# Kernel tuning notes

Measured on AMD Instinct MI355X. Metric: run time of the kernel, lower is better.

The kernel has to match this reference:

```python
import jax, jax.numpy as jnp
import numpy as np

IN_CH, SKIP_CH, OUT_CH = 256, 128, 128
K2 = 9  # 3x3 deformable kernel
LK = 15  # large kernel for offset conv
EPS = 1e-5


def conv2d(x, w, b, pad):
    out = jax.lax.conv_general_dilated(
        x, w, (1, 1), ((pad[0], pad[0]), (pad[1], pad[1])),
        dimension_numbers=("NCHW", "OIHW", "NCHW"))
    return out + b[None, :, None, None]


def conv_transpose_2x2_s2(x, w, b):
    # torch ConvTranspose2d(k=2, s=2, pad=0); w: [in, out, 2, 2]
    wt = jnp.flip(w, (2, 3)).transpose(1, 0, 2, 3)  # [out, in, 2, 2]
    out = jax.lax.conv_general_dilated(
        x, wt, (1, 1), ((1, 1), (1, 1)), lhs_dilation=(2, 2),
        dimension_numbers=("NCHW", "OIHW", "NCHW"))
    return out + b[None, :, None, None]


def bn_relu(x, g, b):
    # training-mode BatchNorm2d (batch statistics) + ReLU
    m = jnp.mean(x, (0, 2, 3), keepdims=True)
    v = jnp.var(x, (0, 2, 3), keepdims=True)
    xn = (x - m) * jax.lax.rsqrt(v + EPS)
    return jax.nn.relu(xn * g[None, :, None, None] + b[None, :, None, None])


def deform_conv3x3(x, offset, mask, w):
    # torchvision DeformConv2d semantics, k=3, stride=1, pad=1, dil=1, no bias
    B, C, H, W = x.shape
    off = offset.reshape(B, K2, 2, H, W)
    dy, dx = off[:, :, 0], off[:, :, 1]            # [B, 9, H, W]
    ki = (jnp.arange(K2) // 3).astype(x.dtype)
    kj = (jnp.arange(K2) % 3).astype(x.dtype)
    hh = jnp.arange(H, dtype=x.dtype)
    ww = jnp.arange(W, dtype=x.dtype)
    y = dy + (hh[None, :, None] + ki[:, None, None] - 1.0)[None]   # [B,9,H,W]
    xx = dx + (ww[None, None, :] + kj[:, None, None] - 1.0)[None]
    y0 = jnp.floor(y)
    x0 = jnp.floor(xx)
    wy = y - y0   # bilinear weights
    wx = xx - x0
    y0i = y0.astype(jnp.int32)
    x0i = x0.astype(jnp.int32)
    x_flat = x.reshape(B, C, H * W)

    def gather(yc, xc):
        valid = ((yc >= 0) & (yc < H) & (xc >= 0) & (xc < W)).astype(x.dtype)
        idx = jnp.clip(yc, 0, H - 1) * W + jnp.clip(xc, 0, W - 1)
        g = jnp.take_along_axis(x_flat, idx.reshape(B, 1, -1), axis=2)
        return g.reshape(B, C, K2, H, W) * valid[:, None]

    v00 = gather(y0i, x0i)
    v01 = gather(y0i, x0i + 1)
    v10 = gather(y0i + 1, x0i)
    v11 = gather(y0i + 1, x0i + 1)
    wye = wy[:, None]
    wxe = wx[:, None]
    sampled = (v00 * (1 - wye) * (1 - wxe) + v01 * (1 - wye) * wxe
               + v10 * wye * (1 - wxe) + v11 * wye * wxe)
    sampled = sampled * mask[:, None]              # [B,C,9,H,W]
    return jnp.einsum("bckhw,ock->bohw", sampled, w.reshape(w.shape[0], C, K2))


def setup_inputs() -> dict:
    key = jax.random.key(0)
    ks = jax.random.split(key, 16)
    s = 0.02
    return {
        "x": jax.random.normal(ks[0], (2, IN_CH, 64, 64), jnp.float32),
        "skip": jax.random.normal(ks[1], (2, SKIP_CH, 128, 128), jnp.float32),
        "w_up": jax.random.normal(ks[2], (IN_CH, OUT_CH, 2, 2), jnp.float32) * s,
        "b_up": jnp.zeros((OUT_CH,), jnp.float32),
        "w_ref": jax.random.normal(ks[3], (OUT_CH, OUT_CH + SKIP_CH, 3, 3), jnp.float32) * s,
        "b_ref": jnp.zeros((OUT_CH,), jnp.float32),
        "g1": jnp.ones((OUT_CH,), jnp.float32),
        "be1": jnp.zeros((OUT_CH,), jnp.float32),
        "w_offh": jax.random.normal(ks[4], (2 * K2, OUT_CH, 1, LK), jnp.float32) * s,
        "b_offh": jnp.zeros((2 * K2,), jnp.float32),
        "w_offv": jax.random.normal(ks[5], (2 * K2, OUT_CH, LK, 1), jnp.float32) * s,
        "b_offv": jnp.zeros((2 * K2,), jnp.float32),
        "w_mask": jax.random.normal(ks[6], (K2, OUT_CH, 3, 3), jnp.float32) * s,
        "b_mask": jnp.zeros((K2,), jnp.float32),
        "w_def": jax.random.normal(ks[7], (OUT_CH, OUT_CH, 3, 3), jnp.float32) * s,
        "g2": jnp.ones((OUT_CH,), jnp.float32),
        "be2": jnp.zeros((OUT_CH,), jnp.float32),
    }


def reference(x, skip, w_up, b_up, w_ref, b_ref, g1, be1,
              w_offh, b_offh, w_offv, b_offv, w_mask, b_mask,
              w_def, g2, be2):
    xu = conv_transpose_2x2_s2(x, w_up, b_up)            # [B, out_ch, 2H, 2W]
    cat = jnp.concatenate([xu, skip], axis=1)
    h = bn_relu(conv2d(cat, w_ref, b_ref, (1, 1)), g1, be1)
    # DSConv: LDoffset = conv(1x15) + conv(15x1); sigmoid mask; deform conv; BN+ReLU
    offset = conv2d(h, w_offh, b_offh, (0, LK // 2)) + conv2d(h, w_offv, b_offv, (LK // 2, 0))
    mask = jax.nn.sigmoid(conv2d(h, w_mask, b_mask, (1, 1)))
    return bn_relu(deform_conv3x3(h, offset, mask, w_def), g2, be2)
```

## Files before the change

### kernel.cpp

```cpp
#include <hip/hip_runtime.h>
#include <hip/hip_bf16.h>

typedef __attribute__((ext_vector_type(8))) short bf16x8;
typedef __attribute__((ext_vector_type(4))) float f32x4;
typedef __attribute__((ext_vector_type(8))) unsigned short u16x8;

static __device__ __forceinline__ unsigned short f2bf(float f) {
  union { float f; unsigned u; } v; v.f = f;
  unsigned r = v.u + 0x7fff + ((v.u >> 16) & 1);
  return (unsigned short)(r >> 16);
}

__global__ void k_wupA(const float* __restrict__ wu, unsigned short* __restrict__ wupA) {
  int idx = blockIdx.x * 256 + threadIdx.x;
  int ic = idx & 255, oc = (idx >> 8) & 127, tap = idx >> 15;
  wupA[idx] = f2bf(wu[(ic * 128 + oc) * 4 + tap]);
}

__global__ __launch_bounds__(256, 2)
void k_upsampleM(const float* __restrict__ x, const unsigned short* __restrict__ wupA,
                 const float* __restrict__ b_up, unsigned short* __restrict__ catT) {
  int bid = blockIdx.x;
  int half = bid & 1;
  int hh = (bid >> 1) & 63;
  int b  = bid >> 7;
  int ww0 = half * 32;
  int t = threadIdx.x;
  int l = t & 63, w = t >> 6;
  int kh = w >> 1, kw = w & 1;
  int lan15 = l & 15, lhi = l >> 4;
  __shared__ unsigned short xs[32][264];

  {
    int ic = t;
    const float4* xp = (const float4*)(x + (((long)(b * 256 + ic)) << 12) + (hh << 6) + ww0);
    #pragma unroll
    for (int q = 0; q < 8; ++q) {
      float4 v = xp[q];
      xs[q * 4 + 0][ic] = f2bf(v.x);
      xs[q * 4 + 1][ic] = f2bf(v.y);
      xs[q * 4 + 2][ic] = f2bf(v.z);
      xs[q * 4 + 3][ic] = f2bf(v.w);
    }
  }
  __syncthreads();

  f32x4 acc[8][2];
  #pragma unroll
  for (int m = 0; m < 8; ++m)
    #pragma unroll
    for (int n = 0; n < 2; ++n)
      #pragma unroll
      for (int r = 0; r < 4; ++r) acc[m][n][r] = 0.f;

  const unsigned short* ab = wupA + ((w * 128 + lan15) << 8) + lhi * 8;
  #pragma unroll
  for (int kc = 0; kc < 8; ++kc) {
    bf16x8 b0 = *(const bf16x8*)(&xs[lan15][kc * 32 + lhi * 8]);
    bf16x8 b1 = *(const bf16x8*)(&xs[16 + lan15][kc * 32 + lhi * 8]);
    #pragma unroll
    for (int mt = 0; mt < 8; ++mt) {
      bf16x8 af = *(const bf16x8*)(ab + (mt << 12) + kc * 32);
      acc[mt][0] = __builtin_amdgcn_mfma_f32_16x16x32_bf16(af, b0, acc[mt][0], 0, 0, 0);
      acc[mt][1] = __builtin_amdgcn_mfma_f32_16x16x32_bf16(af, b1, acc[mt][1], 0, 0, 0);
    }
  }

  int oh = 2 * hh + kh;
  #pragma unroll
  for (int mt = 0; mt < 8; ++mt) {
    int ocb = mt * 16 + lhi * 4;
    float4 bias = *(const float4*)(b_up + ocb);
    int cg = ocb >> 5, icl = ocb & 31;
    long plane = ((long)(b * 8 + cg) << 14) + (oh << 7);
    #pragma unroll
    for (int nt = 0; nt < 2; ++nt) {
      int ow = 2 * (ww0 + nt * 16 + lan15) + kw;
      unsigned u0 = (unsigned)f2bf(acc[mt][nt][0] + bias.x)
                  | ((unsigned)f2bf(acc[mt][nt][1] + bias.y) << 16);
      unsigned u1 = (unsigned)f2bf(acc[mt][nt][2] + bias.z)
                  | ((unsigned)f2bf(acc[mt][nt][3] + bias.w) << 16);
      uint2 pk; pk.x = u0; pk.y = u1;
      *(uint2*)(catT + ((plane + ow) << 5) + icl) = pk;
    }
  }
}

__global__ void k_skipT(const float* __restrict__ skip, unsigned short* __restrict__ catT) {
  int bid = blockIdx.x;
  int xb = bid & 1;
  int y  = (bid >> 1) & 127;
  int cg = (bid >> 8) & 3;
  int b  = bid >> 10;
  int t = threadIdx.x;
  __shared__ float ts[32][65];
  int x = t & 63, c4 = t >> 6, x0 = xb * 64;
  #pragma unroll
  for (int p = 0; p < 8; ++p) {
    int c = p * 4 + c4;
    ts[c][x] = skip[(((long)(b * 128 + cg * 32 + c)) << 14) + (y << 7) + x0 + x];
  }
  __syncthreads();
  int ic = t & 31, xg = t >> 5;
  long plane = ((long)(b * 8 + 4 + cg) << 14) + (y << 7) + x0;
  #pragma unroll
  for (int q = 0; q < 8; ++q) {
    int xx = xg * 8 + q;
    catT[((plane + xx) << 5) + ic] = f2bf(ts[ic][xx]);
  }
}

__global__ void k_wrefT(const float* __restrict__ wr, unsigned short* __restrict__ wbT) {
  int idx = blockIdx.x * 256 + threadIdx.x;
  int tap = idx >> 15;
  int rem = idx & 32767;
  int oc = rem >> 8, ic = rem & 255;
  wbT[idx] = f2bf(wr[(oc * 256 + ic) * 9 + tap]);
}

__global__ void k_womT(const float* __restrict__ wh, const float* __restrict__ wv,
                       const float* __restrict__ wm, unsigned short* __restrict__ wOM) {
  int idx = blockIdx.x * 256 + threadIdx.x;
  int tap = idx / 6144;
  int rem = idx - tap * 6144;
  int j = rem >> 7, ic = rem & 127;
  float v = 0.f;
  if (tap < 15) {
    if (j < 18) v = wh[(j * 128 + ic) * 15 + tap];
  } else if (tap < 30) {
    if (j < 18) v = wv[(j * 128 + ic) * 15 + (tap - 15)];
  } else {
    if (j >= 18 && j < 27) v = wm[((j - 18) * 128 + ic) * 9 + (tap - 30)];
  }
  wOM[idx] = f2bf(v);
}

__global__ void k_wdefA(const float* __restrict__ wd, unsigned short* __restrict__ wdefA) {
  int idx = blockIdx.x * 256 + threadIdx.x;
  if (idx >= 147456) return;
  int j   = idx & 7;
  int oc  = (idx >> 3) & 127;
  int lhi = (idx >> 10) & 3;
  int ks  = idx >> 12;
  int k = ks % 9, cg = ks / 9;
  int c = cg * 32 + lhi * 8 + j;
  wdefA[idx] = f2bf(wd[(oc * 128 + c) * 9 + k]);
}

__global__ __launch_bounds__(512, 2)
void k_conv3w(const unsigned short* __restrict__ catT, const unsigned short* __restrict__ wbT,
              const float* __restrict__ br, float* __restrict__ out) {
  int bid = blockIdx.x;
  int swz = (bid & 7) * 32 + (bid >> 3);
  int y = swz & 127, b = swz >> 7;
  int t = threadIdx.x;
  int l = t & 63, w = t >> 6;
  int ocg = w & 3, xh = w >> 2;
  int oc0 = ocg * 32, px0 = xh * 64;
  int lan15 = l & 15, lhi = l >> 4;
  __shared__ unsigned short xs[3 * 130 * 40];
  const u16x8 z = {0, 0, 0, 0, 0, 0, 0, 0};
  f32x4 acc[2][4];
  #pragma unroll
  for (int m = 0; m < 2; ++m)
    #pragma unroll
    for (int n = 0; n < 4; ++n)
      #pragma unroll
      for (int r = 0; r < 4; ++r) acc[m][n][r] = 0.f;
  const unsigned short* catb = catT + ((long)b << 22);

  #pragma unroll
  for (int it = 0; it < 4; ++it) {
    int idx = it * 512 + t;
    if (idx < 1560) {
      int g = idx & 3, rc = idx >> 2;
      int r = rc / 130, c = rc - r * 130;
      int gy = y + r - 1, gx = c - 1;
      u16x8 v = z;
      if ((unsigned)gy < 128u && (unsigned)gx < 128u)
        v = *(const u16x8*)(catb + (((long)(gy << 7) + gx) << 5) + g * 8);
      *(u16x8*)(xs + (r * 130 + c) * 40 + g * 8) = v;
    }
  }
  __syncthreads();

  for (int cg = 0; cg < 8; ++cg) {
    u16x8 pre[4];
    if (cg < 7) {
      #pragma unroll
      for (int it = 0; it < 4; ++it) {
        int idx = it * 512 + t;
        pre[it] = z;
        if (idx < 1560) {
          int g = idx & 3, rc = idx >> 2;
          int r = rc / 130, c = rc - r * 130;
          int gy = y + r - 1, gx = c - 1;
          if ((unsigned)gy < 128u && (unsigned)gx < 128u)
            pre[it] = *(const u16x8*)(catb + ((((long)(cg + 1) << 14) + (gy << 7) + gx) << 5) + g * 8);
        }
      }
    }
    bf16x8 af[2][9];
    #pragma unroll
    for (int mt = 0; mt < 2; ++mt)
      #pragma unroll
      for (int tap = 0; tap < 9; ++tap)
        af[mt][tap] = *(const bf16x8*)(wbT + ((tap * 128 + oc0 + mt * 16 + lan15) << 8) + cg * 32 + lhi * 8);
    #pragma unroll
    for (int tap = 0; tap < 9; ++tap) {
      int ky = tap / 3, kx = tap % 3;
      #pragma unroll
      for (int nt = 0; nt < 4; ++nt) {
        int c = px0 + nt * 16 + lan15 + kx;
        bf16x8 bfv = *(const bf16x8*)(xs + (ky * 130 + c) * 40 + lhi * 8);
        acc[0][nt] = __builtin_amdgcn_mfma_f32_16x16x32_bf16(af[0][tap], bfv, acc[0][nt], 0, 0, 0);
        acc[1][nt] = __builtin_amdgcn_mfma_f32_16x16x32_bf16(af[1][tap], bfv, acc[1][nt], 0, 0, 0);
      }
    }
    __syncthreads();
    if (cg < 7) {
      #pragma unroll
      for (int it = 0; it < 4; ++it) {
        int idx = it * 512 + t;
        if (idx < 1560) {
          int g = idx & 3, rc = idx >> 2;
          int r = rc / 130, c = rc - r * 130;
          *(u16x8*)(xs + (r * 130 + c) * 40 + g * 8) = pre[it];
        }
      }
      __syncthreads();
    }
  }

  #pragma unroll
  for (int mt = 0; mt < 2; ++mt)
    #pragma unroll
    for (int reg = 0; reg < 4; ++reg) {
      int oc = oc0 + mt * 16 + lhi * 4 + reg;
      float bias = br[oc];
      long obase = ((long)(b * 128 + oc) << 14) + (y << 7) + px0;
      #pragma unroll
      for (int nt = 0; nt < 4; ++nt)
        out[obase + nt * 16 + lan15] = acc[mt][nt][reg] + bias;
    }
}

__global__ void k_bnstats(const float* __restrict__ src, float* __restrict__ mean,
                          float* __restrict__ rstd) {
  int c = blockIdx.x, t = threadIdx.x;
  float s = 0.f, s2 = 0.f;
  for (int b = 0; b < 2; ++b) {
    const float4* p4 = (const float4*)(src + ((long)(b * 128 + c) << 14));
    for (int i = t; i < 4096; i += 256) {
      float4 v = p4[i];
      s  += v.x + v.y + v.z + v.w;
      s2 += v.x * v.x + v.y * v.y + v.z * v.z + v.w * v.w;
    }
  }
  #pragma unroll
  for (int off = 32; off; off >>= 1) {
    s  += __shfl_down(s, off);
    s2 += __shfl_down(s2, off);
  }
  __shared__ float as[4], as2[4];
  int wid = t >> 6;
  if ((t & 63) == 0) { as[wid] = s; as2[wid] = s2; }
  __syncthreads();
  if (t == 0) {
    float S = as[0] + as[1] + as[2] + as[3];
    float S2 = as2[0] + as2[1] + as2[2] + as2[3];
    float m = S / 32768.f;
    float var = S2 / 32768.f - m * m;
    mean[c] = m;
    rstd[c] = rsqrtf(var + 1e-5f);
  }
}

__global__ void k_bnrelu2(const float* __restrict__ tmp1, const float* __restrict__ mean,
                          const float* __restrict__ rstd, const float* __restrict__ g,
                          const float* __restrict__ be, unsigned short* __restrict__ hbufT) {
  int bid = blockIdx.x;
  int xb = bid & 1;
  int y  = (bid >> 1) & 127;
  int cg = (bid >> 8) & 3;
  int b  = bid >> 10;
  int t = threadIdx.x;
  __shared__ float ts[32][65];
  int x = t & 63, c4 = t >> 6, x0 = xb * 64;
  #pragma unroll
  for (int p = 0; p < 8; ++p) {
    int c = p * 4 + c4;
    int ch = cg * 32 + c;
    float sc = rstd[ch] * g[ch];
    float bb = be[ch] - mean[ch] * sc;
    long idx = ((long)(b * 128 + ch) << 14) + (y << 7) + x0 + x;
    ts[c][x] = fmaxf(tmp1[idx] * sc + bb, 0.f);
  }
  __syncthreads();
  int ic = t & 31, xg = t >> 5;
  long plane = ((long)(b * 4 + cg) << 14) + (y << 7) + x0;
  #pragma unroll
  for (int q = 0; q < 8; ++q) {
    int xx = xg * 8 + q;
    hbufT[((plane + xx) << 5) + ic] = f2bf(ts[ic][xx]);
  }
}

__global__ __launch_bounds__(256, 2)
void k_offmasks(const unsigned short* __restrict__ hbufT, const unsigned short* __restrict__ wOM,
                const float* __restrict__ bh, const float* __restrict__ bv,
                const float* __restrict__ bm,
                float* __restrict__ off, float* __restrict__ msk) {
  int bid = blockIdx.x;
  int swz = (bid & 7) * 64 + (bid >> 3);
  int b   = swz >> 8;
  int px0 = (swz & 255) * 64;
  int t = threadIdx.x;
  int l = t & 63, w = t >> 6;
  int lan15 = l & 15, lhi = l >> 4;
  int px = px0 + w * 16;
  int y = px >> 7, x0 = px & 127;
  int x = x0 + lan15;

  __shared__ unsigned short As[4 * 32 * 128];

  f32x4 acc0, acc1;
  #pragma unroll
  for (int r = 0; r < 4; ++r) { acc0[r] = 0.f; acc1[r] = 0.f; }

  const unsigned short* hb = hbufT + ((long)b << 21);
  const u16x8 z = {0, 0, 0, 0, 0, 0, 0, 0};

  for (int grp = 0; grp < 10; ++grp) {
    int tap0 = grp * 4;
    __syncthreads();
    #pragma unroll
    for (int it = 0; it < 8; ++it) {
      int i = it * 256 + t;
      int tl = i >> 9, rem = i & 511;
      int j = rem >> 4, g16 = rem & 15;
      int tap = tap0 + tl;
      u16x8 v = z;
      if (tap < 39) v = *(const u16x8*)(wOM + ((tap * 48 + j) << 7) + g16 * 8);
      *(u16x8*)(As + tl * 4096 + j * 128 + ((g16 ^ (j & 7)) << 3)) = v;
    }
    __syncthreads();
    #pragma unroll
    for (int tl = 0; tl < 4; ++tl) {
      int tap = tap0 + tl;
      if (tap < 39) {
        int ky = (tap < 15) ? 0 : ((tap < 30) ? (tap - 22) : ((tap - 30) / 3 - 1));
        int kx = (tap < 15) ? (tap - 7) : ((tap < 30) ? 0 : ((tap - 30) % 3 - 1));
        int gy = y + ky, gx = x + kx;
        bool valid = ((unsigned)gy < 128u) & ((unsigned)gx < 128u);
        const unsigned short* bp = hb + ((((long)(gy << 7) + gx) << 5) + lhi * 8);
        bool do0 = tap < 30;
        const unsigned short* a0base = As + tl * 4096 + lan15 * 128;
        const unsigned short* a1base = a0base + 16 * 128;
        #pragma unroll
        for (int cg = 0; cg < 4; ++cg) {
          u16x8 bv8 = valid ? *(const u16x8*)(bp + ((long)cg << 19)) : z;
          bf16x8 bf = (bf16x8)bv8;
          int aoff = (((cg << 2) + lhi) ^ (lan15 & 7)) << 3;
          acc1 = __builtin_amdgcn_mfma_f32_16x16x32_bf16(*(const bf16x8*)(a1base + aoff),
                                                         bf, acc1, 0, 0, 0);
          if (do0)
            acc0 = __builtin_amdgcn_mfma_f32_16x16x32_bf16(*(const bf16x8*)(a0base + aoff),
                                                           bf, acc0, 0, 0, 0);
        }
      }
    }
  }

  int sp = (y << 7) + x;
  #pragma unroll
  for (int reg = 0; reg < 4; ++reg) {
    int j0 = lhi * 4 + reg;
    off[((long)(b * 18 + j0) << 14) + sp] = acc0[reg] + bh[j0] + bv[j0];
    int j1 = 16 + lhi * 4 + reg;
    float v = acc1[reg];
    if (j1 < 18) {
      off[((long)(b * 18 + j1) << 14) + sp] = v + bh[j1] + bv[j1];
    } else if (j1 < 27) {
      int jm = j1 - 18;
      msk[((long)(b * 9 + jm) << 14) + sp] = 1.f / (1.f + expf(-(v + bm[jm])));
    }
  }
}

__global__ __launch_bounds__(256, 2)
void k_deformm(const unsigned short* __restrict__ hbufT, const float* __restrict__ off,
               const float* __restrict__ msk, const unsigned short* __restrict__ wdefA,
               float* __restrict__ out) {
  int bid = blockIdx.x;
  int xt = bid & 3;
  int h  = (bid >> 2) & 127;
  int b  = bid >> 9;
  int w0 = xt * 32;
  int t = threadIdx.x;
  int l = t & 63, w = t >> 6;
  int lan15 = l & 15, lhi = l >> 4;

  __shared__ __align__(16) unsigned short S[9][32][40];
  __shared__ int   p_y0[288], p_x0[288];
  __shared__ float p_w00[288], p_w01[288], p_w10[288], p_w11[288];

  for (int idx = t; idx < 288; idx += 256) {
    int k = idx >> 5, pix = idx & 31;
    int sp = (h << 7) + w0 + pix;
    float dy = off[((long)(b * 18 + 2 * k) << 14) + sp];
    float dx = off[((long)(b * 18 + 2 * k + 1) << 14) + sp];
    float m  = msk[((long)(b * 9 + k) << 14) + sp];
    float y  = dy + (float)(h + k / 3 - 1);
    float xx = dx + (float)(w0 + pix + (k % 3) - 1);
    float y0f = floorf(y), x0f = floorf(xx);
    float wy = y - y0f, wx = xx - x0f;
    p_y0[idx] = (int)y0f; p_x0[idx] = (int)x0f;
    p_w00[idx] = (1.f - wy) * (1.f - wx) * m;
    p_w01[idx] = (1.f - wy) * wx * m;
    p_w10[idx] = wy * (1.f - wx) * m;
    p_w11[idx] = wy * wx * m;
  }

  f32x4 acc[2][2];
  #pragma unroll
  for (int m = 0; m < 2; ++m)
    #pragma unroll
    for (int n = 0; n < 2; ++n)
      #pragma unroll
      for (int r = 0; r < 4; ++r) acc[m][n][r] = 0.f;

  for (int cg = 0; cg < 4; ++cg) {
    __syncthreads();
    const unsigned short* hb = hbufT + (((long)(b * 4 + cg)) << 19);
    for (int idx = t; idx < 1152; idx += 256) {
      int cq = idx & 3, pix = (idx >> 2) & 31, k = idx >> 7;
      int kp = (k << 5) + pix;
      int y0 = p_y0[kp], x0 = p_x0[kp];
      float c00 = p_w00[kp], c01 = p_w01[kp], c10 = p_w10[kp], c11 = p_w11[kp];
      bool yi0 = (unsigned)y0 < 128u, yi1 = (unsigned)(y0 + 1) < 128u;
      bool xi0 = (unsigned)x0 < 128u, xi1 = (unsigned)(x0 + 1) < 128u;
      const unsigned short* pbase = hb + ((((long)(y0 << 7) + x0) << 5) + cq * 8);
      u16x8 z = {0, 0, 0, 0, 0, 0, 0, 0};
      u16x8 v00 = (yi0 && xi0) ? *(const u16x8*)pbase          : z;
      u16x8 v01 = (yi0 && xi1) ? *(const u16x8*)(pbase + 32)   : z;
      u16x8 v10 = (yi1 && xi0) ? *(const u16x8*)(pbase + 4096) : z;
      u16x8 v11 = (yi1 && xi1) ? *(const u16x8*)(pbase + 4128) : z;
      u16x8 o;
      #pragma unroll
      for (int j = 0; j < 8; ++j) {
        float s = c00 * __uint_as_float((unsigned)(unsigned short)v00[j] << 16)
                + c01 * __uint_as_float((unsigned)(unsigned short)v01[j] << 16)
                + c10 * __uint_as_float((unsigned)(unsigned short)v10[j] << 16)
                + c11 * __uint_as_float((unsigned)(unsigned short)v11[j] << 16);
        o[j] = f2bf(s);
      }
      *(u16x8*)(&S[k][pix][cq * 8]) = o;
    }
    bf16x8 af0[9], af1[9];
    #pragma unroll
    for (int k = 0; k < 9; ++k) {
      long wbase = ((((long)(cg * 9 + k) * 4 + lhi) * 128) + w * 32 + lan15) * 8;
      af0[k] = *(const bf16x8*)(wdefA + wbase);
      af1[k] = *(const bf16x8*)(wdefA + wbase + 128);
    }
    __syncthreads();
    #pragma unroll
    for (int k = 0; k < 9; ++k) {
      #pragma unroll
      for (int nt = 0; nt < 2; ++nt) {
        bf16x8 bfv = *(const bf16x8*)(&S[k][nt * 16 + lan15][lhi * 8]);
        acc[0][nt] = __builtin_amdgcn_mfma_f32_16x16x32_bf16(af0[k], bfv, acc[0][nt], 0, 0, 0);
        acc[1][nt] = __builtin_amdgcn_mfma_f32_16x16x32_bf16(af1[k], bfv, acc[1][nt], 0, 0, 0);
      }
    }
  }
  #pragma unroll
  for (int mt = 0; mt < 2; ++mt)
    #pragma unroll
    for (int reg = 0; reg < 4; ++reg) {
      int oc = w * 32 + mt * 16 + lhi * 4 + reg;
      long obase = ((long)(b * 128 + oc) << 14) + (h << 7) + w0;
      out[obase + lan15]      = acc[mt][0][reg];
      out[obase + 16 + lan15] = acc[mt][1][reg];
    }
}

__global__ void k_bnrelu(const float4* __restrict__ src, const float* __restrict__ mean,
                         const float* __restrict__ rstd, const float* __restrict__ g,
                         const float* __restrict__ be, float4* __restrict__ dst) {
  int i = blockIdx.x * 256 + threadIdx.x;
  if (i >= 1048576) return;
  int c = (i >> 12) & 127;
  float sc = rstd[c] * g[c];
  float bb = be[c] - mean[c] * sc;
  float4 v = src[i];
  v.x = fmaxf(v.x * sc + bb, 0.f);
  v.y = fmaxf(v.y * sc + bb, 0.f);
  v.z = fmaxf(v.z * sc + bb, 0.f);
  v.w = fmaxf(v.w * sc + bb, 0.f);
  dst[i] = v;
}

extern "C" void kernel_launch(void* const* d_in, const int* in_sizes, int n_in,
                              void* d_out, int out_size, void* d_ws, size_t ws_size,
                              hipStream_t stream) {
  const float* x      = (const float*)d_in[0];
  const float* skip   = (const float*)d_in[1];
  const float* w_up   = (const float*)d_in[2];
  const float* b_up   = (const float*)d_in[3];
  const float* w_ref  = (const float*)d_in[4];
  const float* b_ref  = (const float*)d_in[5];
  const float* g1     = (const float*)d_in[6];
  const float* be1    = (const float*)d_in[7];
  const float* w_offh = (const float*)d_in[8];
  const float* b_offh = (const float*)d_in[9];
  const float* w_offv = (const float*)d_in[10];
  const float* b_offv = (const float*)d_in[11];
  const float* w_mask = (const float*)d_in[12];
  const float* b_mask = (const float*)d_in[13];
  const float* w_def  = (const float*)d_in[14];
  const float* g2     = (const float*)d_in[15];
  const float* be2    = (const float*)d_in[16];

  char* W = (char*)d_ws;
  unsigned short* catT  = (unsigned short*)W;
  float*          tmp1  = (float*)(W + 16777216);
  unsigned short* hbufT = (unsigned short*)(W + 33554432);
  float*          offb  = (float*)(W + 41943040);
  float*          mskb  = (float*)(W + 44302336);
  float*          stat  = (float*)(W + 45481984);
  unsigned short* wbT   = (unsigned short*)(W + 45484032);
  unsigned short* wOM   = (unsigned short*)(W + 46073856);
  unsigned short* wdefA = (unsigned short*)(W + 46553088);
  unsigned short* wupA  = (unsigned short*)(W + 46848000);
  float*          dpre  = (float*)W;

  hipLaunchKernelGGL(k_wrefT, dim3(1152), dim3(256), 0, stream, w_ref, wbT);
  hipLaunchKernelGGL(k_womT, dim3(936), dim3(256), 0, stream, w_offh, w_offv, w_mask, wOM);
  hipLaunchKernelGGL(k_wdefA, dim3(576), dim3(256), 0, stream, w_def, wdefA);
  hipLaunchKernelGGL(k_wupA, dim3(512), dim3(256), 0, stream, w_up, wupA);
  hipLaunchKernelGGL(k_upsampleM, dim3(256), dim3(256), 0, stream, x, wupA, b_up, catT);
  hipLaunchKernelGGL(k_skipT, dim3(2048), dim3(256), 0, stream, skip, catT);
  hipLaunchKernelGGL(k_conv3w, dim3(256), dim3(512), 0, stream, catT, wbT, b_ref, tmp1);
  hipLaunchKernelGGL(k_bnstats, dim3(128), dim3(256), 0, stream, tmp1, stat, stat + 128);
  hipLaunchKernelGGL(k_bnrelu2, dim3(2048), dim3(256), 0, stream, tmp1, stat, stat + 128,
                     g1, be1, hbufT);
  hipLaunchKernelGGL(k_offmasks, dim3(512), dim3(256), 0, stream, hbufT, wOM,
                     b_offh, b_offv, b_mask, offb, mskb);
  hipLaunchKernelGGL(k_deformm, dim3(1024), dim3(256), 0, stream, hbufT, offb, mskb,
                     wdefA, dpre);
  hipLaunchKernelGGL(k_bnstats, dim3(128), dim3(256), 0, stream, dpre, stat + 256, stat + 384);
  hipLaunchKernelGGL(k_bnrelu, dim3(4096), dim3(256), 0, stream,
                     (const float4*)dpre, stat + 256, stat + 384, g2, be2, (float4*)d_out);
}
```

Measured before the change: 184.9 us.

## Split 3x3 refine conv along input channels into two partial-sum outputs

The refine conv kernel now splits the 256 input channels into two halves, launching 512 blocks instead of 256. Each half writes its partial sum to a separate buffer, and the bias is added only in the first half. The BN stats and BN+ReLU kernels are changed to read and sum both partials. The goal is to fill more CUs on the device, since 256 blocks likely underused the GPU. The cost is an extra 16MB fp32 buffer that must be written and then read twice.

```diff
diff --git a/kernel.cpp b/kernel.cpp
--- a/kernel.cpp
+++ b/kernel.cpp
@@ -148,11 +148,14 @@
 }
 
 __global__ __launch_bounds__(512, 2)
-void k_conv3w(const unsigned short* __restrict__ catT, const unsigned short* __restrict__ wbT,
-              const float* __restrict__ br, float* __restrict__ out) {
+void k_conv3s(const unsigned short* __restrict__ catT, const unsigned short* __restrict__ wbT,
+              const float* __restrict__ br, float* __restrict__ out0, float* __restrict__ out1) {
   int bid = blockIdx.x;
-  int swz = (bid & 7) * 32 + (bid >> 3);
-  int y = swz & 127, b = swz >> 7;
+  int swz = (bid & 7) * 64 + (bid >> 3);
+  int kh = swz & 1;
+  int y  = (swz >> 1) & 127;
+  int b  = swz >> 8;
+  int cg0 = kh * 4;
   int t = threadIdx.x;
   int l = t & 63, w = t >> 6;
   int ocg = w & 3, xh = w >> 2;
@@ -178,15 +181,16 @@
       int gy = y + r - 1, gx = c - 1;
       u16x8 v = z;
       if ((unsigned)gy < 128u && (unsigned)gx < 128u)
-        v = *(const u16x8*)(catb + (((long)(gy << 7) + gx) << 5) + g * 8);
+        v = *(const u16x8*)(catb + ((((long)cg0 << 14) + (gy << 7) + gx) << 5) + g * 8);
       *(u16x8*)(xs + (r * 130 + c) * 40 + g * 8) = v;
     }
   }
   __syncthreads();
 
-  for (int cg = 0; cg < 8; ++cg) {
+  for (int ci = 0; ci < 4; ++ci) {
+    int cg = cg0 + ci;
     u16x8 pre[4];
-    if (cg < 7) {
+    if (ci < 3) {
       #pragma unroll
       for (int it = 0; it < 4; ++it) {
         int idx = it * 512 + t;
@@ -218,7 +222,7 @@
       }
     }
     __syncthreads();
-    if (cg < 7) {
+    if (ci < 3) {
       #pragma unroll
       for (int it = 0; it < 4; ++it) {
         int idx = it * 512 + t;
@@ -232,12 +236,13 @@
     }
   }
 
+  float* out = kh ? out1 : out0;
   #pragma unroll
   for (int mt = 0; mt < 2; ++mt)
     #pragma unroll
     for (int reg = 0; reg < 4; ++reg) {
       int oc = oc0 + mt * 16 + lhi * 4 + reg;
-      float bias = br[oc];
+      float bias = kh ? 0.f : br[oc];
       long obase = ((long)(b * 128 + oc) << 14) + (y << 7) + px0;
       #pragma unroll
       for (int nt = 0; nt < 4; ++nt)
@@ -245,16 +250,18 @@
     }
 }
 
-__global__ void k_bnstats(const float* __restrict__ src, float* __restrict__ mean,
-                          float* __restrict__ rstd) {
+__global__ void k_bnstats2(const float* __restrict__ srcA, const float* __restrict__ srcB,
+                           float* __restrict__ mean, float* __restrict__ rstd) {
   int c = blockIdx.x, t = threadIdx.x;
   float s = 0.f, s2 = 0.f;
   for (int b = 0; b < 2; ++b) {
-    const float4* p4 = (const float4*)(src + ((long)(b * 128 + c) << 14));
+    const float4* pa = (const float4*)(srcA + ((long)(b * 128 + c) << 14));
+    const float4* pb = (const float4*)(srcB + ((long)(b * 128 + c) << 14));
     for (int i = t; i < 4096; i += 256) {
-      float4 v = p4[i];
-      s  += v.x + v.y + v.z + v.w;
-      s2 += v.x * v.x + v.y * v.y + v.z * v.z + v.w * v.w;
+      float4 va = pa[i], vb = pb[i];
+      float x0 = va.x + vb.x, x1 = va.y + vb.y, x2 = va.z + vb.z, x3 = va.w + vb.w;
+      s  += x0 + x1 + x2 + x3;
+      s2 += x0 * x0 + x1 * x1 + x2 * x2 + x3 * x3;
     }
   }
   #pragma unroll
@@ -276,9 +283,41 @@
   }
 }
 
-__global__ void k_bnrelu2(const float* __restrict__ tmp1, const float* __restrict__ mean,
-                          const float* __restrict__ rstd, const float* __restrict__ g,
-                          const float* __restrict__ be, unsigned short* __restrict__ hbufT) {
+__global__ void k_bnstats(const float* __restrict__ src, float* __restrict__ mean,
+                          float* __restrict__ rstd) {
+  int c = blockIdx.x, t = threadIdx.x;
+  float s = 0.f, s2 = 0.f;
+  for (int b = 0; b < 2; ++b) {
+    const float4* p4 = (const float4*)(src + ((long)(b * 128 + c) << 14));
+    for (int i = t; i < 4096; i += 256) {
+      float4 v = p4[i];
+      s  += v.x + v.y + v.z + v.w;
+      s2 += v.x * v.x + v.y * v.y + v.z * v.z + v.w * v.w;
+    }
+  }
+  #pragma unroll
+  for (int off = 32; off; off >>= 1) {
+    s  += __shfl_down(s, off);
+    s2 += __shfl_down(s2, off);
+  }
+  __shared__ float as[4], as2[4];
+  int wid = t >> 6;
+  if ((t & 63) == 0) { as[wid] = s; as2[wid] = s2; }
+  __syncthreads();
+  if (t == 0) {
+    float S = as[0] + as[1] + as[2] + as[3];
+    float S2 = as2[0] + as2[1] + as2[2] + as2[3];
+    float m = S / 32768.f;
+    float var = S2 / 32768.f - m * m;
+    mean[c] = m;
+    rstd[c] = rsqrtf(var + 1e-5f);
+  }
+}
+
+__global__ void k_bnrelu2(const float* __restrict__ tA, const float* __restrict__ tB,
+                          const float* __restrict__ mean, const float* __restrict__ rstd,
+                          const float* __restrict__ g, const float* __restrict__ be,
+                          unsigned short* __restrict__ hbufT) {
   int bid = blockIdx.x;
   int xb = bid & 1;
   int y  = (bid >> 1) & 127;
@@ -294,7 +333,7 @@
     float sc = rstd[ch] * g[ch];
     float bb = be[ch] - mean[ch] * sc;
     long idx = ((long)(b * 128 + ch) << 14) + (y << 7) + x0 + x;
-    ts[c][x] = fmaxf(tmp1[idx] * sc + bb, 0.f);
+    ts[c][x] = fmaxf((tA[idx] + tB[idx]) * sc + bb, 0.f);
   }
   __syncthreads();
   int ic = t & 31, xg = t >> 5;
@@ -534,6 +573,7 @@
   unsigned short* wOM   = (unsigned short*)(W + 46073856);
   unsigned short* wdefA = (unsigned short*)(W + 46553088);
   unsigned short* wupA  = (unsigned short*)(W + 46848000);
+  float*          tmp2  = (float*)(W + 47110144);
   float*          dpre  = (float*)W;
 
   hipLaunchKernelGGL(k_wrefT, dim3(1152), dim3(256), 0, stream, w_ref, wbT);
@@ -542,9 +582,9 @@
   hipLaunchKernelGGL(k_wupA, dim3(512), dim3(256), 0, stream, w_up, wupA);
   hipLaunchKernelGGL(k_upsampleM, dim3(256), dim3(256), 0, stream, x, wupA, b_up, catT);
   hipLaunchKernelGGL(k_skipT, dim3(2048), dim3(256), 0, stream, skip, catT);
-  hipLaunchKernelGGL(k_conv3w, dim3(256), dim3(512), 0, stream, catT, wbT, b_ref, tmp1);
-  hipLaunchKernelGGL(k_bnstats, dim3(128), dim3(256), 0, stream, tmp1, stat, stat + 128);
-  hipLaunchKernelGGL(k_bnrelu2, dim3(2048), dim3(256), 0, stream, tmp1, stat, stat + 128,
+  hipLaunchKernelGGL(k_conv3s, dim3(512), dim3(512), 0, stream, catT, wbT, b_ref, tmp1, tmp2);
+  hipLaunchKernelGGL(k_bnstats2, dim3(128), dim3(256), 0, stream, tmp1, tmp2, stat, stat + 128);
+  hipLaunchKernelGGL(k_bnrelu2, dim3(2048), dim3(256), 0, stream, tmp1, tmp2, stat, stat + 128,
                      g1, be1, hbufT);
   hipLaunchKernelGGL(k_offmasks, dim3(512), dim3(256), 0, stream, hbufT, wOM,
                      b_offh, b_offv, b_mask, offb, mskb);
```

Measured after the change: 187.7 us. About the same (+1.5%).
